# Kernel optimization log

Measured on AMD Instinct MI355X. Metric: run time of the kernel, lower is better.

## Reference

```python
import jax, jax.numpy as jnp
import numpy as np


def setup_inputs() -> dict:
    key = jax.random.key(0)
    k1, k2 = jax.random.split(key)
    N, L, Q, H, Lv, P = 1, 6, 300, 8, 4, 4
    # FPN levels for an 800x1333 image at strides 8/16/32/64 (H, W per level)
    spatial_shapes = np.array([[100, 167], [50, 84], [25, 42], [13, 21]], dtype=np.int64)
    level_start_index = np.concatenate([[0], np.cumsum(spatial_shapes.prod(1))[:-1]]).astype(np.int64)
    sampling_locations = jax.random.uniform(k1, (N, L, Q, H, Lv, P, 2), dtype=jnp.float32)
    # attention weights normalized over (levels*points) per head, as MSDeformAttn produces
    aw = jax.random.normal(k2, (N, L, Q, H, Lv, P), dtype=jnp.float32)
    attention_weights = jax.nn.softmax(aw.reshape(N, L, Q, H, Lv * P), axis=-1).reshape(N, L, Q, H, Lv, P)
    return dict(sampling_locations=sampling_locations,
                attention_weights=attention_weights,
                spatial_shapes=spatial_shapes,
                level_start_index=level_start_index)


def reference(sampling_locations, attention_weights, spatial_shapes, level_start_index):
    # sampling_locations: (N, L, Q, H, Lv, P, 2); attention_weights: (N, L, Q, H, Lv, P)
    N, L, Q, H, Lv, P, _ = sampling_locations.shape
    S = int(np.sum(np.asarray(spatial_shapes)[:, 0] * np.asarray(spatial_shapes)[:, 1]))  # static
    ss = jnp.asarray(spatial_shapes)          # (Lv, 2) = (H, W)
    lsi = jnp.asarray(level_start_index)      # (Lv,)

    # permute(0,1,3,2,5,4,6).flatten(0,3) -> (M, P, Lv, 2) with M = N*L*H*Q
    sl = jnp.transpose(sampling_locations, (0, 1, 3, 2, 5, 4, 6)).reshape(-1, P, Lv, 2)
    aw = jnp.transpose(attention_weights, (0, 1, 3, 2, 5, 4)).reshape(-1, P, Lv)
    M = aw.shape[0]

    rev = ss[:, ::-1].astype(sl.dtype)        # (Lv, 2) = (W, H)
    crf = sl * rev                            # float (col, row) coords, (M, P, Lv, 2)
    crll = jnp.floor(crf)
    f = crf - crll                            # fractional part, (M, P, Lv, 2)
    fc, fr = f[..., 0], f[..., 1]

    # corners (d_col, d_row) paired with their bilinear margins (matches torch zipped order)
    offsets = jnp.array([[0, 0], [0, 1], [1, 0], [1, 1]], dtype=jnp.int32)  # ll, lh, hl, hh
    margins = jnp.stack([(fc - 1.0) * (fr - 1.0),   # margin_hh for corner ll
                         -(fc - 1.0) * fr,           # margin_hl for corner lh
                         -fc * (fr - 1.0),           # margin_lh for corner hl
                         fc * fr], axis=0)           # margin_ll for corner hh  -> (4, M, P, Lv)

    cri = crll.astype(jnp.int32)[None] + offsets[:, None, None, None, :]    # (4, M, P, Lv, 2)
    Wlv = ss[:, 1].astype(jnp.int32)
    Hlv = ss[:, 0].astype(jnp.int32)
    valid = ((cri[..., 0] >= 0) & (cri[..., 0] < Wlv) &
             (cri[..., 1] >= 0) & (cri[..., 1] < Hlv))                       # (4, M, P, Lv)

    idx = (cri[..., 1] * Wlv + cri[..., 0] + lsi.astype(jnp.int32)) * valid  # invalid -> 0
    w = aw[None] * valid * margins                                           # invalid -> 0 weight

    # single fused scatter-add over all 4 corners
    idx_flat = jnp.moveaxis(idx, 0, 1).reshape(M, -1)   # (M, 4*P*Lv)
    w_flat = jnp.moveaxis(w, 0, 1).reshape(M, -1)
    rows = jnp.arange(M)[:, None]
    flat_grid = jnp.zeros((M, S), dtype=jnp.float32).at[rows, idx_flat].add(w_flat)

    # torch: reshape(N, Len_q, n_layers, n_heads, -1).sum((2,3)).permute(0,2,1)
    return jnp.transpose(flat_grid.reshape(N, Q, L, H, S).sum(axis=(2, 3)), (0, 2, 1))
```

## Files before the change

kernel.cpp:

```cpp
#include <hip/hip_runtime.h>


constexpr int NQ   = 300;
constexpr int QW   = 8;
constexpr int NG   = 38;
constexpr int NTILES = 21;
constexpr int MAXC = 1280;
constexpr int BLK  = 512;

__global__ __launch_bounds__(BLK, 8)
void msda_tiled(const float4* __restrict__ loc4,
                const float4* __restrict__ aw4,
                float*        __restrict__ out) {
    __shared__ float sm[QW * MAXC];

    const int b  = blockIdx.x;
    const int g  = b / NTILES;
    const int tb = b % NTILES;

    int lv, r0t, nr;
    if (tb < 15)      { lv = 0; r0t = 7  * tb;        nr = min(7,  100 - r0t); }
    else if (tb < 19) { lv = 1; r0t = 15 * (tb - 15); nr = min(15, 50  - r0t); }
    else if (tb < 20) { lv = 2; r0t = 0;              nr = 25; }
    else              { lv = 3; r0t = 0;              nr = 13; }

    const int Wlv_[4] = {167, 84, 42, 21};
    const int Hlv_[4] = {100, 50, 25, 13};
    const int lsi_[4] = {0, 16700, 20900, 21950};
    const int W    = Wlv_[lv];
    const int base = lsi_[lv];
    const int g0   = g * QW;
    const int qw   = min(QW, NQ - g0);
    const int cells = nr * W;
    const int tid  = threadIdx.x;

    {
        const int nz = qw * (MAXC / 4);
        float4* sm4 = (float4*)sm;
        for (int i = tid; i < nz; i += BLK) sm4[i] = make_float4(0.f, 0.f, 0.f, 0.f);
    }
    __syncthreads();

    const int nm  = 48 * qw;
    const int rlo = r0t, rhi = r0t + nr;
    const float fW = (float)W, fH = (float)Hlv_[lv];

    if (tid < nm) {
        const int mi = tid;
        const int m  = 48 * g0 + mi;
        const int ql = mi / 48;
        const int l  = m / 2400;
        const int rem = m - l * 2400;
        const int h  = rem / 300;
        const int q  = rem - h * 300;
        const int t  = (((l * 300 + q) * 8 + h) * 4 + lv) * 4;

        const float4 xy01 = loc4[(t >> 1) + 0];
        const float4 xy23 = loc4[(t >> 1) + 1];
        const float4 w4   = aw4[t >> 2];

        float* smq = &sm[ql * MAXC];

        #pragma unroll
        for (int p = 0; p < 4; ++p) {
            const float x = (p == 0) ? xy01.x : (p == 1) ? xy01.z : (p == 2) ? xy23.x : xy23.z;
            const float y = (p == 0) ? xy01.y : (p == 1) ? xy01.w : (p == 2) ? xy23.y : xy23.w;
            const float w = (p == 0) ? w4.x   : (p == 1) ? w4.y   : (p == 2) ? w4.z   : w4.w;

            const float cf  = x * fW;
            const float rf  = y * fH;
            const float cfl = floorf(cf), rfl = floorf(rf);
            const float fc  = cf - cfl, fr = rf - rfl;
            const int c0 = (int)cfl, rr = (int)rfl;
            const int c1 = c0 + 1, r1 = rr + 1;

            const bool cv0 = (unsigned)c0 < (unsigned)W;
            const bool cv1 = (unsigned)c1 < (unsigned)W;
            const bool rv0 = (rr >= rlo) & (rr < rhi);
            const bool rv1 = (r1 >= rlo) & (r1 < rhi);

            const float omfc = 1.0f - fc, omfr = 1.0f - fr;
            if (rv0) {
                const int ro = (rr - rlo) * W;
                if (cv0) atomicAdd(&smq[ro + c0], w * omfc * omfr);
                if (cv1) atomicAdd(&smq[ro + c1], w * fc   * omfr);
            }
            if (rv1) {
                const int ro = (r1 - rlo) * W;
                if (cv0) atomicAdd(&smq[ro + c0], w * omfc * fr);
                if (cv1) atomicAdd(&smq[ro + c1], w * fc   * fr);
            }
        }
    }
    __syncthreads();

    const int s0  = base + r0t * W;
    const int nq4 = qw >> 2;
    for (int i = tid; i < cells * nq4; i += BLK) {
        const int cell = i / nq4;
        const int v    = i - cell * nq4;
        float4 val;
        val.x = sm[(v * 4 + 0) * MAXC + cell];
        val.y = sm[(v * 4 + 1) * MAXC + cell];
        val.z = sm[(v * 4 + 2) * MAXC + cell];
        val.w = sm[(v * 4 + 3) * MAXC + cell];
        *(float4*)&out[(s0 + cell) * NQ + g0 + v * 4] = val;
    }
}

extern "C" void kernel_launch(void* const* d_in, const int* in_sizes, int n_in,
                              void* d_out, int out_size, void* d_ws, size_t ws_size,
                              hipStream_t stream) {
    const float4* loc4 = (const float4*)d_in[0];
    const float4* aw4  = (const float4*)d_in[1];
    float* out = (float*)d_out;

    msda_tiled<<<NG * NTILES, BLK, 0, stream>>>(loc4, aw4, out);
}
```

Baseline: 80.61 us.

## Pre-bin bilinear samples into per-tile record lists before shared-memory accumulation

A new pre-pass computes every sampling point once and appends a compact record (cell, query slot, row weight, column fraction) to a per-tile bin in global workspace, using global atomic counters. A separate kernel zeroes those counters first. The tile kernel then reads only the records that land in its row range, instead of having every tile block re-read and filter all samples for its level. This adds two extra launches, global atomic contention and workspace traffic. Bins are capped at a fixed record capacity, so any bin that overflows would silently drop records.

```diff
diff --git a/kernel.cpp b/kernel.cpp
--- a/kernel.cpp
+++ b/kernel.cpp
@@ -1,17 +1,97 @@
 #include <hip/hip_runtime.h>
 
 
-constexpr int NQ   = 300;
-constexpr int QW   = 8;
-constexpr int NG   = 38;
+constexpr int NQ     = 300;
+constexpr int QW     = 8;
+constexpr int NG     = 38;
 constexpr int NTILES = 21;
-constexpr int MAXC = 1280;
-constexpr int BLK  = 512;
+constexpr int MAXC   = 1280;
+constexpr int BLK    = 512;
+constexpr int MTOT   = 14400;
+constexpr int NBINS  = NG * NTILES;
+constexpr int CAP    = 3072;
+constexpr int CNTSTRIDE = 16;
+
+__global__ __launch_bounds__(256)
+void msda_zero(unsigned int* __restrict__ cnt) {
+    const int i = blockIdx.x * 256 + threadIdx.x;
+    if (i < NBINS * CNTSTRIDE) cnt[i] = 0u;
+}
+
+__global__ __launch_bounds__(256, 8)
+void msda_bin(const float4* __restrict__ loc4,
+              const float4* __restrict__ aw4,
+              float4*       __restrict__ recs,
+              unsigned int* __restrict__ cnt) {
+    const int tid = blockIdx.x * 256 + threadIdx.x;
+    const int lv = tid & 3;
+    const int s  = tid >> 2;
+    const int l  = s / 2400;
+    const int rem = s - l * 2400;
+    const int q  = rem >> 3;
+    const int h  = rem & 7;
+    const int m  = (l * 8 + h) * 300 + q;
+    const int g  = m / 384;
+    const unsigned ql = (unsigned)((m / 48) & 7);
+
+    const int W = (lv == 0) ? 167 : (lv == 1) ? 84 : (lv == 2) ? 42 : 21;
+    const int H = (lv == 0) ? 100 : (lv == 1) ? 50 : (lv == 2) ? 25 : 13;
+    const float fW = (float)W, fH = (float)H;
+
+    const float4 xy01 = loc4[2 * tid];
+    const float4 xy23 = loc4[2 * tid + 1];
+    const float4 w4   = aw4[tid];
+
+    const int binbase = g * NTILES;
+
+    #pragma unroll
+    for (int p = 0; p < 4; ++p) {
+        const float x = (p == 0) ? xy01.x : (p == 1) ? xy01.z : (p == 2) ? xy23.x : xy23.z;
+        const float y = (p == 0) ? xy01.y : (p == 1) ? xy01.w : (p == 2) ? xy23.y : xy23.w;
+        const float w = (p == 0) ? w4.x   : (p == 1) ? w4.y   : (p == 2) ? w4.z   : w4.w;
+
+        const float cf  = x * fW;
+        const float rf  = y * fH;
+        const float cfl = floorf(cf), rfl = floorf(rf);
+        const float fc  = cf - cfl, fr = rf - rfl;
+        const int c0 = (int)cfl, rr = (int)rfl;
+
+        const unsigned cv0 = (unsigned)c0 < (unsigned)W;
+        const unsigned cv1 = (unsigned)(c0 + 1) < (unsigned)W;
+        if (!(cv0 | cv1)) continue;
+
+        #pragma unroll
+        for (int e = 0; e < 2; ++e) {
+            const int r = rr + e;
+            if ((unsigned)r >= (unsigned)H) continue;
+            int tb, r0t;
+            if (lv == 0)      { tb = r / 7;            r0t = 7  * (r / 7);  }
+            else if (lv == 1) { const int t = r / 15;  tb = 15 + t; r0t = 15 * t; }
+            else if (lv == 2) { tb = 19; r0t = 0; }
+            else              { tb = 20; r0t = 0; }
+
+            const float wrow = w * (e ? fr : (1.0f - fr));
+            const int cellbase = (r - r0t) * W + c0;
+            const unsigned meta = (cv1 << 21) | (cv0 << 20) | (ql << 16)
+                                | (unsigned)(cellbase + 1);
+            const int bin = binbase + tb;
+            const unsigned idx = atomicAdd(&cnt[bin * CNTSTRIDE], 1u);
+            if (idx < CAP) {
+                float4 rec;
+                rec.x = __int_as_float((int)meta);
+                rec.y = wrow;
+                rec.z = fc;
+                rec.w = 0.f;
+                recs[(size_t)bin * CAP + idx] = rec;
+            }
+        }
+    }
+}
 
 __global__ __launch_bounds__(BLK, 8)
-void msda_tiled(const float4* __restrict__ loc4,
-                const float4* __restrict__ aw4,
-                float*        __restrict__ out) {
+void msda_tiled(const float4* __restrict__ recs,
+                const unsigned int* __restrict__ cnt,
+                float* __restrict__ out) {
     __shared__ float sm[QW * MAXC];
 
     const int b  = blockIdx.x;
@@ -25,7 +105,6 @@
     else              { lv = 3; r0t = 0;              nr = 13; }
 
     const int Wlv_[4] = {167, 84, 42, 21};
-    const int Hlv_[4] = {100, 50, 25, 13};
     const int lsi_[4] = {0, 16700, 20900, 21950};
     const int W    = Wlv_[lv];
     const int base = lsi_[lv];
@@ -34,6 +113,10 @@
     const int cells = nr * W;
     const int tid  = threadIdx.x;
 
+    const int bin = g * NTILES + tb;
+    const int n   = min((int)cnt[bin * CNTSTRIDE], CAP);
+    const float4* myrec = recs + (size_t)bin * CAP;
+
     {
         const int nz = qw * (MAXC / 4);
         float4* sm4 = (float4*)sm;
@@ -41,56 +124,14 @@
     }
     __syncthreads();
 
-    const int nm  = 48 * qw;
-    const int rlo = r0t, rhi = r0t + nr;
-    const float fW = (float)W, fH = (float)Hlv_[lv];
-
-    if (tid < nm) {
-        const int mi = tid;
-        const int m  = 48 * g0 + mi;
-        const int ql = mi / 48;
-        const int l  = m / 2400;
-        const int rem = m - l * 2400;
-        const int h  = rem / 300;
-        const int q  = rem - h * 300;
-        const int t  = (((l * 300 + q) * 8 + h) * 4 + lv) * 4;
-
-        const float4 xy01 = loc4[(t >> 1) + 0];
-        const float4 xy23 = loc4[(t >> 1) + 1];
-        const float4 w4   = aw4[t >> 2];
-
-        float* smq = &sm[ql * MAXC];
-
-        #pragma unroll
-        for (int p = 0; p < 4; ++p) {
-            const float x = (p == 0) ? xy01.x : (p == 1) ? xy01.z : (p == 2) ? xy23.x : xy23.z;
-            const float y = (p == 0) ? xy01.y : (p == 1) ? xy01.w : (p == 2) ? xy23.y : xy23.w;
-            const float w = (p == 0) ? w4.x   : (p == 1) ? w4.y   : (p == 2) ? w4.z   : w4.w;
-
-            const float cf  = x * fW;
-            const float rf  = y * fH;
-            const float cfl = floorf(cf), rfl = floorf(rf);
-            const float fc  = cf - cfl, fr = rf - rfl;
-            const int c0 = (int)cfl, rr = (int)rfl;
-            const int c1 = c0 + 1, r1 = rr + 1;
-
-            const bool cv0 = (unsigned)c0 < (unsigned)W;
-            const bool cv1 = (unsigned)c1 < (unsigned)W;
-            const bool rv0 = (rr >= rlo) & (rr < rhi);
-            const bool rv1 = (r1 >= rlo) & (r1 < rhi);
-
-            const float omfc = 1.0f - fc, omfr = 1.0f - fr;
-            if (rv0) {
-                const int ro = (rr - rlo) * W;
-                if (cv0) atomicAdd(&smq[ro + c0], w * omfc * omfr);
-                if (cv1) atomicAdd(&smq[ro + c1], w * fc   * omfr);
-            }
-            if (rv1) {
-                const int ro = (r1 - rlo) * W;
-                if (cv0) atomicAdd(&smq[ro + c0], w * omfc * fr);
-                if (cv1) atomicAdd(&smq[ro + c1], w * fc   * fr);
-            }
-        }
+    for (int i = tid; i < n; i += BLK) {
+        const float4 rec = myrec[i];
+        const unsigned meta = (unsigned)__float_as_int(rec.x);
+        const int cell = (int)(meta & 0xFFFFu) - 1;
+        float* smq = &sm[((meta >> 16) & 7u) * MAXC];
+        const float wrow = rec.y, fc = rec.z;
+        if (meta & (1u << 20)) atomicAdd(&smq[cell],     wrow * (1.0f - fc));
+        if (meta & (1u << 21)) atomicAdd(&smq[cell + 1], wrow * fc);
     }
     __syncthreads();
 
@@ -115,5 +156,10 @@
     const float4* aw4  = (const float4*)d_in[1];
     float* out = (float*)d_out;
 
-    msda_tiled<<<NG * NTILES, BLK, 0, stream>>>(loc4, aw4, out);
+    float4* recs = (float4*)d_ws;
+    unsigned int* cnt = (unsigned int*)((char*)d_ws + (size_t)NBINS * CAP * 16);
+
+    msda_zero<<<(NBINS * CNTSTRIDE + 255) / 256, 256, 0, stream>>>(cnt);
+    msda_bin<<<(MTOT * 4) / 256, 256, 0, stream>>>(loc4, aw4, recs, cnt);
+    msda_tiled<<<NG * NTILES, BLK, 0, stream>>>(recs, cnt, out);
 }
```

New measurement: 153.7 us. 90.7% more time.
